# Optimization experiments

Measured on AMD Instinct MI355X. Metric: run time of the kernel, lower is better.

Reference implementation:

```python
import jax, jax.numpy as jnp
import numpy as np

NDIM = 3
N = 192
DX = 1.0 / N          # uniform unit box
T_REF = 300.0         # reference temperature [K]
MU_REF = 1.8e-5       # reference viscosity [Pa s]
PR = 0.72             # Prandtl number
CP = 1005.0           # specific heat [J/kg/K]


def _ddx(f, axis):
    # 2nd-order central difference, periodic BC
    return (jnp.roll(f, -1, axis) - jnp.roll(f, 1, axis)) / (2.0 * DX)


def _gradient(f):
    # scalar [N,N,N] -> [NDIM, N,N,N]
    return jnp.stack([_ddx(f, a) for a in range(NDIM)], axis=0)


def _divergence(v):
    # vector [NDIM, N,N,N] -> [N,N,N]
    out = _ddx(v[0], 0)
    for a in range(1, NDIM):
        out = out + _ddx(v[a], a)
    return out


def _viscosity(T_dim):
    return MU_REF * (T_dim / T_REF) ** 0.7


def _conductivity(T_dim):
    return _viscosity(T_dim) * CP / PR


def setup_inputs() -> dict:
    key = jax.random.key(0)
    k1, k2 = jax.random.split(key)
    u = jax.random.normal(k1, (NDIM, N, N, N), dtype=jnp.float32)
    # nondimensional temperature, kept positive for the power-law viscosity
    T = jax.random.uniform(k2, (N, N, N), dtype=jnp.float32, minval=0.5, maxval=1.5)
    return {"u": u, "T": T}


def reference(u, T):
    # --- stress tensor ---
    mu = _viscosity(T * T_REF)                                   # [N,N,N]
    # gradu[i, j] = d u_i / d x_j
    gradu = jnp.stack([_gradient(u[i]) for i in range(NDIM)], 0)  # [3,3,N,N,N]
    divu = jnp.einsum('ii...->...', gradu)                        # trace -> [N,N,N]
    S = 0.5 * (gradu + jnp.swapaxes(gradu, 0, 1))                 # symmetrized
    eye = jnp.eye(NDIM, dtype=u.dtype)[:, :, None, None, None]
    tau = 2.0 * mu * S - (2.0 / 3.0) * mu * divu * eye            # [3,3,N,N,N]

    # --- heat flux ---
    k = _conductivity(T * T_REF)
    heat_flux = -k * _gradient(T)                                 # [3,N,N,N]

    # --- assemble RHS: [mass(=0), momentum(3), energy] ---
    momentum = jnp.stack([_divergence(tau[i]) for i in range(NDIM)], 0)
    energy = -_divergence(heat_flux)
    for i in range(NDIM):
        energy = energy + _divergence(tau[i] * u[i])
    zero = jnp.zeros_like(T)
    return jnp.concatenate([zero[None], momentum, energy[None]], axis=0)
```

## Files before the change

### kernel.cpp

```cpp
#include <hip/hip_runtime.h>

#define N  192
#define N2 (N * N)
#define N3 (N * N * N)

#define TX 32
#define TY 8
#define NT 256
#define ZC 12
#define GX (N / TX)
#define GY (N / TY)
#define GZ (N / ZC)
#define NBLK (GX * GY * GZ)
#define UX (TX + 4)
#define UY (TY + 4)
#define UP (UX * UY)
#define FX (TX + 2)
#define FY (TY + 2)
#define FP (FX * FY)

static constexpr float INV2DX     = (float)N / 2.0f;
static constexpr float SCALE2     = INV2DX * INV2DX;
static constexpr float MU_REF_F   = 1.8e-5f;
static constexpr float CP_OVER_PR = 1005.0f / 0.72f;
static constexpr float TWO_THIRDS = 2.0f / 3.0f;

__device__ __forceinline__ int wrapN(int a) {
    if (a < 0)  a += N;
    if (a >= N) a -= N;
    return a;
}

struct Flux { float t00, t01, t02, t11, t12, t22, F0, F1, F2; };

__device__ __forceinline__ Flux flux_eval(const float4* __restrict__ uM,
                                          const float4* __restrict__ uC,
                                          const float4* __restrict__ uP,
                                          int c)
{
    const float4 cc = uC[c];
    const float4 xp = uC[c + 1],  xm = uC[c - 1];
    const float4 yp = uC[c + UX], ym = uC[c - UX];
    const float4 zp = uP[c],      zm = uM[c];

    const float d00 = zp.x - zm.x;
    const float d01 = yp.x - ym.x;
    const float d02 = xp.x - xm.x;
    const float d10 = zp.y - zm.y;
    const float d11 = yp.y - ym.y;
    const float d12 = xp.y - xm.y;
    const float d20 = zp.z - zm.z;
    const float d21 = yp.z - ym.z;
    const float d22 = xp.z - xm.z;
    const float dT0 = zp.w - zm.w;
    const float dT1 = yp.w - ym.w;
    const float dT2 = xp.w - xm.w;

    const float mu   = MU_REF_F * __powf(cc.w, 0.7f);
    const float mu2  = mu + mu;
    const float divu = d00 + d11 + d22;
    const float lam  = -TWO_THIRDS * mu * divu;

    Flux f;
    f.t00 = mu2 * d00 + lam;
    f.t11 = mu2 * d11 + lam;
    f.t22 = mu2 * d22 + lam;
    f.t01 = mu * (d01 + d10);
    f.t02 = mu * (d02 + d20);
    f.t12 = mu * (d12 + d21);
    const float kc = mu * CP_OVER_PR;
    f.F0 = kc * dT0 + f.t00 * cc.x + f.t01 * cc.y + f.t02 * cc.z;
    f.F1 = kc * dT1 + f.t01 * cc.x + f.t11 * cc.y + f.t12 * cc.z;
    f.F2 = kc * dT2 + f.t02 * cc.x + f.t12 * cc.y + f.t22 * cc.z;
    return f;
}

__device__ __forceinline__ void sf_store(float4* __restrict__ sA, float4* __restrict__ sB,
                                         int fi, const Flux& f)
{
    sA[fi] = make_float4(f.t01, f.t02, f.t11, f.t12);
    sB[fi] = make_float4(f.t22, f.F1,  f.F2,  0.0f);
}

__global__ __launch_bounds__(NT)
void diffusion_zmarch_kernel(const float* __restrict__ u,
                             const float* __restrict__ Tp,
                             float* __restrict__ out)
{
    __shared__ float4 su4[4][UP];
    __shared__ float4 sfA[2][FP];
    __shared__ float4 sfB[2][FP];

    const int id  = (int)blockIdx.x;
    const int nid = (id & 7) * (NBLK / 8) + (id >> 3);
    const int bzB = nid / (GX * GY);
    const int rem = nid % (GX * GY);
    const int bx  = (rem % GX) * TX;
    const int by  = (rem / GX) * TY;
    const int z0  = bzB * ZC;

    const int tx  = threadIdx.x & (TX - 1);
    const int ty  = threadIdx.x >> 5;
    const int tid = (int)threadIdx.x;

    const float* __restrict__ u0 = u;
    const float* __restrict__ u1 = u + N3;
    const float* __restrict__ u2 = u + 2 * N3;

    const int cu = (ty + 2) * UX + (tx + 2);
    const int fi = (ty + 1) * FX + (tx + 1);

    int hfx = -1, hfy = -1;
    if (tid < TX)                 { hfy = 0;      hfx = 1 + tid; }
    else if (tid < 2 * TX)        { hfy = FY - 1; hfx = 1 + tid - TX; }
    else if (tid < 2 * TX + TY)   { hfx = 0;      hfy = 1 + tid - 2 * TX; }
    else if (tid < 2 * (TX + TY)) { hfx = FX - 1; hfy = 1 + tid - 2 * TX - TY; }
    const int hcu = (hfy + 1) * UX + (hfx + 1);
    const int hfi = hfy * FX + hfx;

    const int  q0   = tid;
    const int  q1   = tid + NT;
    const bool has2 = (q1 < UP);
    int ro0, ro1 = 0;
    {
        const int ux = q0 % UX, uy = q0 / UX;
        ro0 = wrapN(by + uy - 2) * N + wrapN(bx + ux - 2);
    }
    if (has2) {
        const int ux = q1 % UX, uy = q1 / UX;
        ro1 = wrapN(by + uy - 2) * N + wrapN(bx + ux - 2);
    }

#define STAGE_DIRECT(slot, zw)                                              \
    do {                                                                    \
        const int base_ = (zw) * N2;                                        \
        {  const int g_ = base_ + ro0;                                      \
           su4[slot][q0] = make_float4(u0[g_], u1[g_], u2[g_], Tp[g_]); }   \
        if (has2) {                                                         \
           const int g_ = base_ + ro1;                                      \
           su4[slot][q1] = make_float4(u0[g_], u1[g_], u2[g_], Tp[g_]); }   \
    } while (0)

    STAGE_DIRECT(0, wrapN(z0 - 2));
    STAGE_DIRECT(1, wrapN(z0 - 1));
    STAGE_DIRECT(2, z0);
    STAGE_DIRECT(3, z0 + 1);
    __syncthreads();

    float t00m, t01m, t02m, F0m;
    float t00c, t01c, t02c, F0c;
    {
        const Flux fM = flux_eval(su4[0], su4[1], su4[2], cu);
        t00m = fM.t00; t01m = fM.t01; t02m = fM.t02; F0m = fM.F0;
        const Flux fC = flux_eval(su4[1], su4[2], su4[3], cu);
        t00c = fC.t00; t01c = fC.t01; t02c = fC.t02; F0c = fC.F0;
        sf_store(sfA[0], sfB[0], fi, fC);
        if (hfx >= 0) {
            const Flux h = flux_eval(su4[1], su4[2], su4[3], hcu);
            sf_store(sfA[0], sfB[0], hfi, h);
        }
    }
    __syncthreads();
    STAGE_DIRECT(0, z0 + 2);
    __syncthreads();

    float4 *pM = su4[2], *pC = su4[3], *pP = su4[0], *pW = su4[1];
    int cur = 1;

    int idx = z0 * N2 + (by + ty) * N + bx + tx;
    int zw  = z0 + 3; if (zw >= N) zw -= N;

    for (int it = 0; it < ZC; ++it) {
        const bool pref = (it <= ZC - 2);
        float4 r0, r1;
        if (pref) {
            const int base_ = zw * N2;
            { const int g_ = base_ + ro0;
              r0 = make_float4(u0[g_], u1[g_], u2[g_], Tp[g_]); }
            if (has2) {
              const int g_ = base_ + ro1;
              r1 = make_float4(u0[g_], u1[g_], u2[g_], Tp[g_]); }
        }

        const Flux fp_ = flux_eval(pM, pC, pP, cu);
        Flux h;
        if (hfx >= 0) h = flux_eval(pM, pC, pP, hcu);

        const float4* __restrict__ sA = sfA[cur ^ 1];
        const float4* __restrict__ sB = sfB[cur ^ 1];
        const float4 ayp = sA[fi + FX], aym = sA[fi - FX];
        const float4 axp = sA[fi + 1],  axm = sA[fi - 1];
        const float4 byp = sB[fi + FX], bym = sB[fi - FX];
        const float4 bxp = sB[fi + 1],  bxm = sB[fi - 1];

        const float m0 = (fp_.t00 - t00m) + (ayp.x - aym.x) + (axp.y - axm.y);
        const float m1 = (fp_.t01 - t01m) + (ayp.z - aym.z) + (axp.w - axm.w);
        const float m2 = (fp_.t02 - t02m) + (ayp.w - aym.w) + (bxp.x - bxm.x);
        const float en = (fp_.F0  - F0m)  + (byp.y - bym.y) + (bxp.z - bxm.z);

        out[idx]          = 0.0f;
        out[1 * N3 + idx] = m0 * SCALE2;
        out[2 * N3 + idx] = m1 * SCALE2;
        out[3 * N3 + idx] = m2 * SCALE2;
        out[4 * N3 + idx] = en * SCALE2;

        if (pref) { pW[q0] = r0; if (has2) pW[q1] = r1; }
        sf_store(sfA[cur], sfB[cur], fi, fp_);
        if (hfx >= 0) sf_store(sfA[cur], sfB[cur], hfi, h);

        __syncthreads();

        t00m = t00c; t01m = t01c; t02m = t02c; F0m = F0c;
        t00c = fp_.t00; t01c = fp_.t01; t02c = fp_.t02; F0c = fp_.F0;
        float4* t = pM; pM = pC; pC = pP; pP = pW; pW = t;
        cur ^= 1;
        idx += N2;
        if (++zw >= N) zw = 0;
    }
#undef STAGE_DIRECT
}

extern "C" void kernel_launch(void* const* d_in, const int* in_sizes, int n_in,
                              void* d_out, int out_size, void* d_ws, size_t ws_size,
                              hipStream_t stream)
{
    const float* u   = (const float*)d_in[0];
    const float* T   = (const float*)d_in[1];
    float*       out = (float*)d_out;

    hipLaunchKernelGGL(diffusion_zmarch_kernel, dim3(NBLK), dim3(NT), 0, stream,
                       u, T, out);
}
```

Baseline: 105.5 us.

## Keep z-neighbour values in registers and repack flux LDS by direction

The z-march now carries each thread's z-minus and centre values (and its halo point's) in registers, so the stencil ring in shared memory shrinks from four planes to three and each step does fewer LDS reads. The flux shared arrays are repacked so the y-direction and x-direction flux components each sit in one float4, cutting neighbour flux reads from eight float4 loads to four. The prologue gains an extra staging phase and barrier, and the extra live float4 registers may raise register pressure.

Measured after the change: 105.2 us. About the same (-0.3%).

```diff
diff --git a/kernel.cpp b/kernel.cpp
--- a/kernel.cpp
+++ b/kernel.cpp
@@ -33,15 +33,12 @@
 
 struct Flux { float t00, t01, t02, t11, t12, t22, F0, F1, F2; };
 
-__device__ __forceinline__ Flux flux_eval(const float4* __restrict__ uM,
-                                          const float4* __restrict__ uC,
-                                          const float4* __restrict__ uP,
-                                          int c)
-{
-    const float4 cc = uC[c];
+__device__ __forceinline__ Flux flux_eval_reg(const float4 zm, const float4 cc,
+                                              const float4 zp,
+                                              const float4* __restrict__ uC, int c)
+{
     const float4 xp = uC[c + 1],  xm = uC[c - 1];
     const float4 yp = uC[c + UX], ym = uC[c - UX];
-    const float4 zp = uP[c],      zm = uM[c];
 
     const float d00 = zp.x - zm.x;
     const float d01 = yp.x - ym.x;
@@ -75,11 +72,18 @@
     return f;
 }
 
-__device__ __forceinline__ void sf_store(float4* __restrict__ sA, float4* __restrict__ sB,
+__device__ __forceinline__ Flux flux_eval_lds(const float4* __restrict__ uM,
+                                              const float4* __restrict__ uC,
+                                              const float4* __restrict__ uP, int c)
+{
+    return flux_eval_reg(uM[c], uC[c], uP[c], uC, c);
+}
+
+__device__ __forceinline__ void sf_store(float4* __restrict__ sY, float4* __restrict__ sX,
                                          int fi, const Flux& f)
 {
-    sA[fi] = make_float4(f.t01, f.t02, f.t11, f.t12);
-    sB[fi] = make_float4(f.t22, f.F1,  f.F2,  0.0f);
+    sY[fi] = make_float4(f.t01, f.t11, f.t12, f.F1);
+    sX[fi] = make_float4(f.t02, f.t12, f.t22, f.F2);
 }
 
 __global__ __launch_bounds__(NT)
@@ -87,9 +91,9 @@
                              const float* __restrict__ Tp,
                              float* __restrict__ out)
 {
-    __shared__ float4 su4[4][UP];
-    __shared__ float4 sfA[2][FP];
-    __shared__ float4 sfB[2][FP];
+    __shared__ float4 su4[3][UP];
+    __shared__ float4 sfY[2][FP];
+    __shared__ float4 sfX[2][FP];
 
     const int id  = (int)blockIdx.x;
     const int nid = (id & 7) * (NBLK / 8) + (id >> 3);
@@ -115,6 +119,7 @@
     else if (tid < 2 * TX)        { hfy = FY - 1; hfx = 1 + tid - TX; }
     else if (tid < 2 * TX + TY)   { hfx = 0;      hfy = 1 + tid - 2 * TX; }
     else if (tid < 2 * (TX + TY)) { hfx = FX - 1; hfy = 1 + tid - 2 * TX - TY; }
+    const bool hasH = (hfx >= 0);
     const int hcu = (hfy + 1) * UX + (hfx + 1);
     const int hfi = hfy * FX + hfx;
 
@@ -144,27 +149,37 @@
     STAGE_DIRECT(0, wrapN(z0 - 2));
     STAGE_DIRECT(1, wrapN(z0 - 1));
     STAGE_DIRECT(2, z0);
-    STAGE_DIRECT(3, z0 + 1);
     __syncthreads();
 
     float t00m, t01m, t02m, F0m;
+    {
+        const Flux fM = flux_eval_lds(su4[0], su4[1], su4[2], cu);
+        t00m = fM.t00; t01m = fM.t01; t02m = fM.t02; F0m = fM.F0;
+    }
+    __syncthreads();
+    STAGE_DIRECT(0, z0 + 1);
+    __syncthreads();
+
     float t00c, t01c, t02c, F0c;
     {
-        const Flux fM = flux_eval(su4[0], su4[1], su4[2], cu);
-        t00m = fM.t00; t01m = fM.t01; t02m = fM.t02; F0m = fM.F0;
-        const Flux fC = flux_eval(su4[1], su4[2], su4[3], cu);
+        const Flux fC = flux_eval_lds(su4[1], su4[2], su4[0], cu);
         t00c = fC.t00; t01c = fC.t01; t02c = fC.t02; F0c = fC.F0;
-        sf_store(sfA[0], sfB[0], fi, fC);
-        if (hfx >= 0) {
-            const Flux h = flux_eval(su4[1], su4[2], su4[3], hcu);
-            sf_store(sfA[0], sfB[0], hfi, h);
+        sf_store(sfY[0], sfX[0], fi, fC);
+        if (hasH) {
+            const Flux h = flux_eval_lds(su4[1], su4[2], su4[0], hcu);
+            sf_store(sfY[0], sfX[0], hfi, h);
         }
     }
     __syncthreads();
-    STAGE_DIRECT(0, z0 + 2);
-    __syncthreads();
-
-    float4 *pM = su4[2], *pC = su4[3], *pP = su4[0], *pW = su4[1];
+    STAGE_DIRECT(1, z0 + 2);
+    __syncthreads();
+
+    float4 rzm = su4[2][cu];
+    float4 rcc = su4[0][cu];
+    float4 hzm, hcc;
+    if (hasH) { hzm = su4[2][hcu]; hcc = su4[0][hcu]; }
+
+    float4 *pC = su4[0], *pP = su4[1], *pW = su4[2];
     int cur = 1;
 
     int idx = z0 * N2 + (by + ty) * N + bx + tx;
@@ -182,21 +197,23 @@
               r1 = make_float4(u0[g_], u1[g_], u2[g_], Tp[g_]); }
         }
 
-        const Flux fp_ = flux_eval(pM, pC, pP, cu);
-        Flux h;
-        if (hfx >= 0) h = flux_eval(pM, pC, pP, hcu);
-
-        const float4* __restrict__ sA = sfA[cur ^ 1];
-        const float4* __restrict__ sB = sfB[cur ^ 1];
-        const float4 ayp = sA[fi + FX], aym = sA[fi - FX];
-        const float4 axp = sA[fi + 1],  axm = sA[fi - 1];
-        const float4 byp = sB[fi + FX], bym = sB[fi - FX];
-        const float4 bxp = sB[fi + 1],  bxm = sB[fi - 1];
-
-        const float m0 = (fp_.t00 - t00m) + (ayp.x - aym.x) + (axp.y - axm.y);
-        const float m1 = (fp_.t01 - t01m) + (ayp.z - aym.z) + (axp.w - axm.w);
-        const float m2 = (fp_.t02 - t02m) + (ayp.w - aym.w) + (bxp.x - bxm.x);
-        const float en = (fp_.F0  - F0m)  + (byp.y - bym.y) + (bxp.z - bxm.z);
+        const float4 own = pP[cu];
+        const Flux fp_ = flux_eval_reg(rzm, rcc, own, pC, cu);
+        float4 hown; Flux h;
+        if (hasH) {
+            hown = pP[hcu];
+            h = flux_eval_reg(hzm, hcc, hown, pC, hcu);
+        }
+
+        const float4* __restrict__ sY = sfY[cur ^ 1];
+        const float4* __restrict__ sX = sfX[cur ^ 1];
+        const float4 yp = sY[fi + FX], ym = sY[fi - FX];
+        const float4 xp = sX[fi + 1],  xm = sX[fi - 1];
+
+        const float m0 = (fp_.t00 - t00m) + (yp.x - ym.x) + (xp.x - xm.x);
+        const float m1 = (fp_.t01 - t01m) + (yp.y - ym.y) + (xp.y - xm.y);
+        const float m2 = (fp_.t02 - t02m) + (yp.z - ym.z) + (xp.z - xm.z);
+        const float en = (fp_.F0  - F0m)  + (yp.w - ym.w) + (xp.w - xm.w);
 
         out[idx]          = 0.0f;
         out[1 * N3 + idx] = m0 * SCALE2;
@@ -205,14 +222,16 @@
         out[4 * N3 + idx] = en * SCALE2;
 
         if (pref) { pW[q0] = r0; if (has2) pW[q1] = r1; }
-        sf_store(sfA[cur], sfB[cur], fi, fp_);
-        if (hfx >= 0) sf_store(sfA[cur], sfB[cur], hfi, h);
+        sf_store(sfY[cur], sfX[cur], fi, fp_);
+        if (hasH) sf_store(sfY[cur], sfX[cur], hfi, h);
 
         __syncthreads();
 
         t00m = t00c; t01m = t01c; t02m = t02c; F0m = F0c;
         t00c = fp_.t00; t01c = fp_.t01; t02c = fp_.t02; F0c = fp_.F0;
-        float4* t = pM; pM = pC; pC = pP; pP = pW; pW = t;
+        rzm = rcc; rcc = own;
+        if (hasH) { hzm = hcc; hcc = hown; }
+        float4* t = pC; pC = pP; pP = pW; pW = t;
         cur ^= 1;
         idx += N2;
         if (++zw >= N) zw = 0;
```
